# Optimization experiments

Hardware: AMD Instinct MI355X
Metric: run time of the kernel (lower is better)

Reference implementation:

```python
import jax, jax.numpy as jnp
import numpy as np

DIM = 1024
NUM_HEADS = 8
HEAD_DIM = 64
QK_DIM = NUM_HEADS * HEAD_DIM  # 512
B, S = 4, 1024


def setup_inputs() -> dict:
    key = jax.random.key(0)
    k1, k2, k3, k4, k5 = jax.random.split(key, 5)
    x = jax.random.normal(k1, (B, S, DIM), dtype=jnp.float32)
    mask = jax.random.randint(k2, (B, S), 0, 2).astype(bool)
    rotator = jax.random.normal(k3, (B, S, HEAD_DIM, HEAD_DIM), dtype=jnp.float32)
    # Linear weights stored as [in, out] for x @ W
    w_t = jax.random.normal(k4, (DIM, 2 * QK_DIM + DIM), dtype=jnp.float32) * (DIM ** -0.5)
    w_o = jax.random.normal(k5, (DIM, DIM), dtype=jnp.float32) * (DIM ** -0.5)
    return {"x": x, "mask": mask, "rotator": rotator, "w_t": w_t, "w_o": w_o}


def taylor_atn_fn(qs, ks, vs, mask):
    # 2nd-order Taylor approximation of softmax attention:
    # exp(s) ~= 1 + s + s^2/2, with invalid keys masked out.
    scale = HEAD_DIM ** -0.5
    s = jnp.einsum('bqhd,bkhd->bhqk', qs, ks) * scale  # [B,H,S,S]
    scores = 1.0 + s + 0.5 * s * s
    scores = scores * mask[:, None, None, :].astype(scores.dtype)  # mask keys
    denom = jnp.maximum(jnp.sum(scores, axis=-1), 1e-6)            # [B,H,Q]
    out = jnp.einsum('bhqk,bkhd->bqhd', scores, vs)
    out = out / jnp.transpose(denom, (0, 2, 1))[..., None]         # [B,Q,H,vd]
    return out.reshape(out.shape[0], out.shape[1], -1)


def reference(x, mask, rotator, w_t, w_o):
    t = x @ w_t                                   # [B,S,2*QK+DIM]
    Bx, Sx = t.shape[0], t.shape[1]
    qs = t[..., :QK_DIM].reshape(Bx, Sx, NUM_HEADS, HEAD_DIM)
    ks = t[..., QK_DIM:2 * QK_DIM].reshape(Bx, Sx, NUM_HEADS, HEAD_DIM)
    vs = t[..., 2 * QK_DIM:].reshape(Bx, Sx, NUM_HEADS, -1)
    m = mask[..., None, None]
    # masked per-position rotation: q -> R q, k -> R^T k
    qs = jnp.where(m, jnp.einsum('bsij,bshj->bshi', rotator, qs), qs)
    ks = jnp.where(m, jnp.einsum('bsij,bshi->bshj', rotator, ks), ks)
    out = taylor_atn_fn(qs, ks, vs, mask)
    return out @ w_o
```

## Files before the change

### kernel.cpp

```cpp
#include <hip/hip_runtime.h>
#include <cstdint>
#include <cstddef>

#define DIMX  1024
#define NH    8
#define HD    64
#define QKD   512
#define VDD   128
#define BATCH 4
#define SEQ   1024
#define NPOS  (BATCH*SEQ)
#define TW    (2*QKD + DIMX)
#define SCALE 0.125f

typedef __bf16 bf16x8 __attribute__((ext_vector_type(8)));
typedef float  f32x4  __attribute__((ext_vector_type(4)));
typedef float  f32x16 __attribute__((ext_vector_type(16)));

__device__ __forceinline__ ushort f2bf(float f) {
    unsigned b = __float_as_uint(f);
    return (ushort)((b + 0x7FFFu + ((b >> 16) & 1u)) >> 16);
}
__device__ __forceinline__ float bf2f(ushort u) {
    return __uint_as_float((unsigned)u << 16);
}

__device__ __forceinline__ unsigned cvtpk(float lo, float hi) {
    unsigned r;
    asm("v_cvt_pk_bf16_f32 %0, %1, %2" : "=v"(r) : "v"(lo), "v"(hi));
    return r;
}

__device__ __forceinline__ void plswap(unsigned &a, unsigned &b) {
    asm("v_permlane32_swap_b32 %0, %1" : "+v"(a), "+v"(b));
}

#define GLD16(src, dst) __builtin_amdgcn_global_load_lds(                      \
    (const __attribute__((address_space(1))) unsigned int*)(src),              \
    (__attribute__((address_space(3))) unsigned int*)(dst), 16, 0, 0)

#define SW(row, col) ((row)*64 + ((col) ^ (((row)&7)<<3)))

__device__ __forceinline__ int2 xcd_swz(int gx, int gy) {
    const int nwg = gx * gy;
    int id = blockIdx.y * gx + blockIdx.x;
    id = (id & 7) * (nwg >> 3) + (id >> 3);
    return make_int2(id % gx, id / gx);
}

__global__ __launch_bounds__(256)
void prep_all(const float* __restrict__ x, const float* __restrict__ w_t,
              const float* __restrict__ w_o, ushort* __restrict__ xbf,
              ushort* __restrict__ wtT, ushort* __restrict__ woT)
{
    __shared__ float tile[32][33];
    const int bid = blockIdx.x;
    if (bid < 2048) {
        const size_t i = ((size_t)bid * 256 + threadIdx.x) * 8;
        float4 v0 = *(const float4*)(x + i);
        float4 v1 = *(const float4*)(x + i + 4);
        ushort o[8] = {f2bf(v0.x), f2bf(v0.y), f2bf(v0.z), f2bf(v0.w),
                       f2bf(v1.x), f2bf(v1.y), f2bf(v1.z), f2bf(v1.w)};
        *(uint4*)(xbf + i) = *(uint4*)o;
        return;
    }
    const float* W; ushort* WT; int K, N, bn, bk;
    if (bid < 4096) {
        W = w_t; WT = wtT; K = DIMX; N = TW;
        const int t = bid - 2048;
        bn = (t & 63) * 32; bk = (t >> 6) * 32;
    } else {
        W = w_o; WT = woT; K = DIMX; N = DIMX;
        const int t = bid - 4096;
        bn = (t & 31) * 32; bk = (t >> 5) * 32;
    }
    const int tx = threadIdx.x & 31;
    const int ty = threadIdx.x >> 5;
    #pragma unroll
    for (int i = ty; i < 32; i += 8)
        tile[i][tx] = W[(size_t)(bk + i) * N + bn + tx];
    __syncthreads();
    #pragma unroll
    for (int i = ty; i < 32; i += 8)
        WT[(size_t)(bn + i) * K + bk + tx] = f2bf(tile[tx][i]);
}

#define GEMM_PROLOGUE(Aptr, Bptr, Kdim)                                        \
    __shared__ __align__(16) ushort lA[128 * 64];                              \
    __shared__ __align__(16) ushort lB[128 * 64];                              \
    const int tid  = threadIdx.x;                                              \
    const int lane = tid & 63;                                                 \
    const int wave = tid >> 6;                                                 \
    const int wr   = wave >> 1;                                                \
    const int wc   = wave & 1;                                                 \
    const int rsub = lane >> 3;                        \
    const int scol = ((lane & 7) * 8) ^ ((rsub & 7) << 3);                     \
    const ushort* aP = (Aptr) + (size_t)(bm + wave*32 + rsub) * (Kdim) + scol; \
    const ushort* bP = (Bptr) + (size_t)(bn + wave*32 + rsub) * (Kdim) + scol; \
    ushort* lAw = lA + wave * 2048;                                            \
    ushort* lBw = lB + wave * 2048;                                            \
    const int fr = lane & 15;                                                  \
    const int l4 = lane >> 4;                                                  \
    f32x4 acc[4][4] = {};

#define GEMM_KLOOP(Kdim)                                                       \
    for (int k0 = 0; k0 < (Kdim); k0 += 64) {                                  \
        _Pragma("unroll")                                                      \
        for (int c = 0; c < 4; ++c) {                                          \
            GLD16(aP + (size_t)(c*8) * (Kdim) + k0, lAw + c*512);              \
            GLD16(bP + (size_t)(c*8) * (Kdim) + k0, lBw + c*512);              \
        }                                                                      \
        asm volatile("s_waitcnt vmcnt(0)" ::: "memory");                       \
        __syncthreads();                                                       \
        _Pragma("unroll")                                                      \
        for (int ks = 0; ks < 2; ++ks) {                                       \
            bf16x8 af[4], bfr[4];                                              \
            _Pragma("unroll")                                                  \
            for (int m = 0; m < 4; ++m)                                        \
                af[m] = *(const bf16x8*)&lA[SW(wr*64 + m*16 + fr,              \
                                               ks*32 + l4*8)];                 \
            _Pragma("unroll")                                                  \
            for (int n = 0; n < 4; ++n)                                        \
                bfr[n] = *(const bf16x8*)&lB[SW(wc*64 + n*16 + fr,             \
                                                ks*32 + l4*8)];               \
            _Pragma("unroll")                                                  \
            for (int m = 0; m < 4; ++m)                                        \
                _Pragma("unroll")                                              \
                for (int n = 0; n < 4; ++n)                                    \
                    acc[m][n] = __builtin_amdgcn_mfma_f32_16x16x32_bf16(       \
                        af[m], bfr[n], acc[m][n], 0, 0, 0);                    \
        }                                                                      \
        __syncthreads();                                                       \
    }

__global__ __launch_bounds__(256, 2)
void gemm_qkv(const ushort* __restrict__ A, const ushort* __restrict__ BT,
              ushort* __restrict__ t1b, ushort* __restrict__ Vt)
{
    const int2 bij = xcd_swz(TW/128, NPOS/128);
    const int bm = bij.y * 128;
    const int bn = bij.x * 128;
    GEMM_PROLOGUE(A, BT, DIMX)
    GEMM_KLOOP(DIMX)

    const int orow = l4 * 4;
    if (bn < 1024) {
        #pragma unroll
        for (int m = 0; m < 4; ++m)
            #pragma unroll
            for (int n = 0; n < 4; ++n) {
                ushort* dst = t1b + (size_t)(bm + wr * 64 + m * 16 + orow) * 1024
                                  + bn + wc * 64 + n * 16 + fr;
                #pragma unroll
                for (int q = 0; q < 4; ++q)
                    dst[(size_t)q * 1024] = f2bf(acc[m][n][q]);
            }
    } else {
        #pragma unroll
        for (int m = 0; m < 4; ++m)
            #pragma unroll
            for (int n = 0; n < 4; ++n) {
                const int row0 = bm + wr * 64 + m * 16 + orow;
                const int cv   = bn + wc * 64 + n * 16 + fr - 1024;
                const int hh = cv >> 7, vd = cv & 127;
                const int bb = row0 >> 10, ss = row0 & 1023;
                ushort o4[4];
                #pragma unroll
                for (int q = 0; q < 4; ++q) o4[q] = f2bf(acc[m][n][q]);
                *(ushort4*)&Vt[((size_t)(bb*NH + hh)*VDD + vd)*SEQ + ss] =
                    *(ushort4*)o4;
            }
    }
}

__global__ __launch_bounds__(256, 2)
void gemm_bf16_mfma(const ushort* __restrict__ A, const ushort* __restrict__ BT,
                    float* __restrict__ C)
{
    const int2 bij = xcd_swz(DIMX/128, NPOS/128);
    const int bm = bij.y * 128;
    const int bn = bij.x * 128;
    GEMM_PROLOGUE(A, BT, DIMX)
    GEMM_KLOOP(DIMX)

    const int orow = l4 * 4;
    #pragma unroll
    for (int m = 0; m < 4; ++m)
        #pragma unroll
        for (int n = 0; n < 4; ++n) {
            float* dst = C + (size_t)(bm + wr * 64 + m * 16 + orow) * DIMX
                           + bn + wc * 64 + n * 16 + fr;
            #pragma unroll
            for (int q = 0; q < 4; ++q)
                dst[(size_t)q * DIMX] = acc[m][n][q];
        }
}

__global__ __launch_bounds__(256)
void rotate_pack_qk(const ushort* __restrict__ t1b, const int* __restrict__ mask,
                    const float* __restrict__ rot, ushort* __restrict__ Qb,
                    ushort* __restrict__ Kb)
{
    const int p   = blockIdx.x;
    const int tid = threadIdx.x;
    const int b = p >> 10, s = p & 1023;
    const bool rotated = (mask[p] != 0);

    __shared__ float R[64][69];
    __shared__ float qv[QKD];
    __shared__ float kv[QKD];

    const ushort* tq = t1b + (size_t)p * 1024;
    {
        ushort2 q2 = *(const ushort2*)(tq + tid*2);
        ushort2 k2 = *(const ushort2*)(tq + QKD + tid*2);
        qv[tid*2]   = bf2f(q2.x); qv[tid*2+1] = bf2f(q2.y);
        kv[tid*2]   = bf2f(k2.x); kv[tid*2+1] = bf2f(k2.y);
        if (rotated) {
            const float* Rg = rot + (size_t)p * 4096;
            const int base = tid * 16;
            const int r = base >> 6, c = base & 63;
            #pragma unroll
            for (int x = 0; x < 16; x += 4) {
                float4 v = *(const float4*)(Rg + base + x);
                R[r][c+x+0] = v.x; R[r][c+x+1] = v.y;
                R[r][c+x+2] = v.z; R[r][c+x+3] = v.w;
            }
        }
    }
    __syncthreads();

    #pragma unroll
    for (int ph = 0; ph < 2; ++ph) {
        const int h = (tid >> 6) + ph*4;
        const int i = tid & 63;
        const float* qh  = &qv[h*64];
        const float* kh2 = &kv[h*64];
        float aq, ak;
        if (rotated) {
            aq = 0.f; ak = 0.f;
            #pragma unroll 8
            for (int j = 0; j < 64; ++j) {
                aq = fmaf(R[i][j], qh[j], aq);
                ak = fmaf(R[j][i], kh2[j], ak);
            }
        } else {
            aq = qh[i]; ak = kh2[i];
        }
        const size_t dst = ((size_t)(b*NH + h)*SEQ + s)*HD + i;
        Qb[dst] = f2bf(aq * SCALE);
        Kb[dst] = f2bf(ak);
    }
}

__global__ __launch_bounds__(256, 2)
void taylor_attn_mfma(const ushort* __restrict__ Qb, const ushort* __restrict__ Kb,
                      const ushort* __restrict__ Vt, const int* __restrict__ mask,
                      ushort* __restrict__ attn)
{
    const int bh  = blockIdx.x;
    const int qt  = blockIdx.y;
    const int b   = bh >> 3, h = bh & 7;
    const int tid = threadIdx.x;
    const int lane = tid & 63;
    const int wave = tid >> 6;
    const int kh  = wave >> 1;
    const int qg  = wave & 1;
    const int l31 = lane & 31;
    const int g   = lane >> 5;

    __shared__ __align__(16) ushort smem[32768];
    __shared__ float mskAll[SEQ];
    __shared__ float dpart[64];
    __shared__ float dinv2[64];

    ushort* Ksp = smem + kh * 8192;
    ushort* Vsp = smem + 16384 + kh * 8192;
    float*  comb = (float*)smem;

    {
        int4 mv = *(const int4*)(mask + b*SEQ + tid*4);
        float4 f = make_float4(mv.x ? 1.f : 0.f, mv.y ? 1.f : 0.f,
                               mv.z ? 1.f : 0.f, mv.w ? 1.f : 0.f);
        *(float4*)&mskAll[tid*4] = f;
    }

    const ushort* qrow = Qb + ((size_t)bh*SEQ + qt*64 + qg*32 + l31) * HD + g*8;
    bf16x8 qf[4];
    #pragma unroll
    for (int ds = 0; ds < 4; ++ds) qf[ds] = *(const bf16x8*)(qrow + ds*16);

    const int sub  = lane >> 3;
    const int scol = ((lane & 7) * 8) ^ (sub << 3);
    const ushort* Kbase = Kb + (size_t)bh*SEQ*HD;
    const ushort* Vbase = Vt + (size_t)bh*VDD*SEQ;

#define ISSUE_K(buf, ktn) do {                                                 \
    _Pragma("unroll")                                                          \
    for (int i_ = 0; i_ < 4; ++i_)                                             \
        GLD16(Kbase + ((size_t)(ktn)*64 + 8*(qg*4+i_) + sub)*HD + scol,        \
              Ksp + (buf)*4096 + (qg*4+i_)*512);                               \
} while (0)
#define ISSUE_V(ktn) do {                                                      \
    _Pragma("unroll")                                                          \
    for (int i_ = 0; i_ < 8; ++i_)                                             \
        GLD16(Vbase + (size_t)(8*(qg*8+i_) + sub)*SEQ + (ktn)*64 + scol,       \
              Vsp + (qg*8+i_)*512);                                            \
} while (0)

    f32x16 acc[4] = {};
    float dacc = 0.f;

    __syncthreads();
    ISSUE_K(0, kh*8);

    for (int it = 0; it < 8; ++it) {
        const int kt = kh*8 + it;
        const int cb = it & 1;
        ISSUE_V(kt);
        if (it < 7) {
            ISSUE_K(cb ^ 1, kt + 1);
            asm volatile("s_waitcnt vmcnt(12)" ::: "memory");
        } else {
            asm volatile("s_waitcnt vmcnt(8)"  ::: "memory");
        }
        __builtin_amdgcn_s_barrier();

        f32x16 sf0 = {}, sf1 = {};
        __builtin_amdgcn_s_setprio(1);
        #pragma unroll
        for (int ds = 0; ds < 4; ++ds) {
            const int dc = ds*16 + g*8;
            bf16x8 kf0 = *(const bf16x8*)&Ksp[cb*4096 + SW(l31, dc)];
            bf16x8 kf1 = *(const bf16x8*)&Ksp[cb*4096 + SW(32 + l31, dc)];
            sf0 = __builtin_amdgcn_mfma_f32_32x32x16_bf16(kf0, qf[ds], sf0, 0, 0, 0);
            sf1 = __builtin_amdgcn_mfma_f32_32x32x16_bf16(kf1, qf[ds], sf1, 0, 0, 0);
        }
        __builtin_amdgcn_s_setprio(0);

        const float* mrow = mskAll + kt*64;
        unsigned w0[8], w1[8];
        float dadd = 0.f;
        #pragma unroll
        for (int rr = 0; rr < 4; ++rr) {
            const float4 mqa = *(const float4*)&mrow[8*rr + 4*g];
            const float4 mqb = *(const float4*)&mrow[32 + 8*rr + 4*g];
            float s0 = sf0[rr*4+0], s1 = sf0[rr*4+1];
            float s2 = sf0[rr*4+2], s3 = sf0[rr*4+3];
            float c0 = fmaf(fmaf(0.5f*s0, s0, s0), mqa.x, mqa.x);
            float c1 = fmaf(fmaf(0.5f*s1, s1, s1), mqa.y, mqa.y);
            float c2 = fmaf(fmaf(0.5f*s2, s2, s2), mqa.z, mqa.z);
            float c3 = fmaf(fmaf(0.5f*s3, s3, s3), mqa.w, mqa.w);
            float t0 = sf1[rr*4+0], t1 = sf1[rr*4+1];
            float t2 = sf1[rr*4+2], t3 = sf1[rr*4+3];
            float d0 = fmaf(fmaf(0.5f*t0, t0, t0), mqb.x, mqb.x);
            float d1 = fmaf(fmaf(0.5f*t1, t1, t1), mqb.y, mqb.y);
            float d2 = fmaf(fmaf(0.5f*t2, t2, t2), mqb.z, mqb.z);
            float d3 = fmaf(fmaf(0.5f*t3, t3, t3), mqb.w, mqb.w);
            dadd += ((c0+c1)+(c2+c3)) + ((d0+d1)+(d2+d3));
            w0[rr*2+0] = cvtpk(c0, c1);
            w0[rr*2+1] = cvtpk(c2, c3);
            w1[rr*2+0] = cvtpk(d0, d1);
            w1[rr*2+1] = cvtpk(d2, d3);
        }
        dacc += dadd;
        plswap(w0[0], w0[2]); plswap(w0[1], w0[3]);
        plswap(w0[4], w0[6]); plswap(w0[5], w0[7]);
        plswap(w1[0], w1[2]); plswap(w1[1], w1[3]);
        plswap(w1[4], w1[6]); plswap(w1[5], w1[7]);

        if (it < 7) asm volatile("s_waitcnt vmcnt(4)" ::: "memory");
        else        asm volatile("s_waitcnt vmcnt(0)" ::: "memory");
        __builtin_amdgcn_s_barrier();

        __builtin_amdgcn_s_setprio(1);
        #pragma unroll
        for (int kq = 0; kq < 4; ++kq) {
            union { unsigned u[4]; bf16x8 v; } pu;
            if (kq == 0)      { pu.u[0]=w0[0]; pu.u[1]=w0[1]; pu.u[2]=w0[2]; pu.u[3]=w0[3]; }
            else if (kq == 1) { pu.u[0]=w0[4]; pu.u[1]=w0[5]; pu.u[2]=w0[6]; pu.u[3]=w0[7]; }
            else if (kq == 2) { pu.u[0]=w1[0]; pu.u[1]=w1[1]; pu.u[2]=w1[2]; pu.u[3]=w1[3]; }
            else              { pu.u[0]=w1[4]; pu.u[1]=w1[5]; pu.u[2]=w1[6]; pu.u[3]=w1[7]; }
            const int kcol = kq*16 + g*8;
            acc[0] = __builtin_amdgcn_mfma_f32_32x32x16_bf16(
                pu.v, *(const bf16x8*)&Vsp[SW(      l31, kcol)], acc[0], 0, 0, 0);
            acc[1] = __builtin_amdgcn_mfma_f32_32x32x16_bf16(
                pu.v, *(const bf16x8*)&Vsp[SW( 32 + l31, kcol)], acc[1], 0, 0, 0);
            acc[2] = __builtin_amdgcn_mfma_f32_32x32x16_bf16(
                pu.v, *(const bf16x8*)&Vsp[SW( 64 + l31, kcol)], acc[2], 0, 0, 0);
            acc[3] = __builtin_amdgcn_mfma_f32_32x32x16_bf16(
                pu.v, *(const bf16x8*)&Vsp[SW( 96 + l31, kcol)], acc[3], 0, 0, 0);
        }
        __builtin_amdgcn_s_setprio(0);
        __builtin_amdgcn_s_barrier();
    }
#undef ISSUE_K
#undef ISSUE_V

    const float dhalf = dacc + __shfl_xor(dacc, 32);

    if (kh == 1) {
        float* cbp = comb + qg * 4096;
        #pragma unroll
        for (int vb = 0; vb < 4; ++vb)
            #pragma unroll
            for (int rr = 0; rr < 4; ++rr) {
                float4 v = make_float4(acc[vb][rr*4+0], acc[vb][rr*4+1],
                                       acc[vb][rr*4+2], acc[vb][rr*4+3]);
                *(float4*)&cbp[(vb*32 + l31)*32 + 4*g + 8*rr] = v;
            }
        if (lane < 32) dpart[qg*32 + l31] = dhalf;
    }
    __syncthreads();
    if (kh == 0) {
        float* cbp = comb + qg * 4096;
        const float dtot = dhalf + dpart[qg*32 + l31];
        if (lane < 32) dinv2[qg*32 + l31] = 1.f / fmaxf(dtot, 1e-6f);
        #pragma unroll
        for (int vb = 0; vb < 4; ++vb)
            #pragma unroll
            for (int rr = 0; rr < 4; ++rr) {
                float4 v = *(const float4*)&cbp[(vb*32 + l31)*32 + 4*g + 8*rr];
                acc[vb][rr*4+0] += v.x; acc[vb][rr*4+1] += v.y;
                acc[vb][rr*4+2] += v.z; acc[vb][rr*4+3] += v.w;
            }
        float inv[16];
        #pragma unroll
        for (int rr = 0; rr < 4; ++rr) {
            float4 iv = *(const float4*)&dinv2[qg*32 + 8*rr + 4*g];
            inv[rr*4+0] = iv.x; inv[rr*4+1] = iv.y;
            inv[rr*4+2] = iv.z; inv[rr*4+3] = iv.w;
        }
        ushort* obase = attn + ((size_t)(b*SEQ + qt*64 + qg*32)) * DIMX
                      + h*VDD + l31;
        #pragma unroll
        for (int vb = 0; vb < 4; ++vb)
            #pragma unroll
            for (int rr = 0; rr < 4; ++rr)
                #pragma unroll
                for (int j = 0; j < 4; ++j) {
                    const int q = 4*g + 8*rr + j;
                    obase[(size_t)q*DIMX + vb*32] = f2bf(acc[vb][rr*4+j] * inv[rr*4+j]);
                }
    }
}

extern "C" void kernel_launch(void* const* d_in, const int* in_sizes, int n_in,
                              void* d_out, int out_size, void* d_ws, size_t ws_size,
                              hipStream_t stream)
{
    const float* x    = (const float*)d_in[0];
    const int*   mask = (const int*)d_in[1];
    const float* rot  = (const float*)d_in[2];
    const float* w_t  = (const float*)d_in[3];
    const float* w_o  = (const float*)d_in[4];
    float* out = (float*)d_out;

    ushort* t1b    = (ushort*)d_ws;
    ushort* xbf    = t1b + (size_t)NPOS * 1024;
    ushort* attnbf = xbf;
    ushort* wtT    = xbf + (size_t)NPOS * DIMX;
    ushort* woT    = wtT + (size_t)TW * DIMX;
    ushort* Qb     = woT + (size_t)DIMX * DIMX;
    ushort* Kb     = Qb  + (size_t)BATCH * NH * SEQ * HD;
    ushort* Vtp    = Kb  + (size_t)BATCH * NH * SEQ * HD;

    prep_all<<<5120, 256, 0, stream>>>(x, w_t, w_o, xbf, wtT, woT);

    gemm_qkv<<<dim3(TW/128, NPOS/128), 256, 0, stream>>>(xbf, wtT, t1b, Vtp);
    rotate_pack_qk<<<NPOS, 256, 0, stream>>>(t1b, mask, rot, Qb, Kb);
    taylor_attn_mfma<<<dim3(BATCH*NH, SEQ/64), 256, 0, stream>>>(Qb, Kb, Vtp, mask, attnbf);
    gemm_bf16_mfma<<<dim3(DIMX/128, NPOS/128), 256, 0, stream>>>(attnbf, woT, out);
}
```

Before: 98.34 us.

## Give each wave private K/V LDS tiles to remove per-iteration workgroup barriers

Result: slower. 101.4 us (+3.2%).

```diff
diff --git a/kernel.cpp b/kernel.cpp
--- a/kernel.cpp
+++ b/kernel.cpp
@@ -40,6 +40,7 @@
     (__attribute__((address_space(3))) unsigned int*)(dst), 16, 0, 0)
 
 #define SW(row, col) ((row)*64 + ((col) ^ (((row)&7)<<3)))
+#define SW32(row, col) ((row)*32 + ((col) ^ ((((row)>>1)&3)<<3)))
 
 __device__ __forceinline__ int2 xcd_swz(int gx, int gy) {
     const int nwg = gx * gy;
@@ -274,8 +275,8 @@
     __shared__ float dpart[64];
     __shared__ float dinv2[64];
 
-    ushort* Ksp = smem + kh * 8192;
-    ushort* Vsp = smem + 16384 + kh * 8192;
+    ushort* Ksp = smem + wave * 8192;
+    ushort* Vsp = Ksp + 4096;
     float*  comb = (float*)smem;
 
     {
@@ -290,114 +291,99 @@
     #pragma unroll
     for (int ds = 0; ds < 4; ++ds) qf[ds] = *(const bf16x8*)(qrow + ds*16);
 
-    const int sub  = lane >> 3;
-    const int scol = ((lane & 7) * 8) ^ (sub << 3);
+    const int ksub  = lane >> 3;
+    const int kcolS = ((lane & 7) * 8) ^ (ksub << 3);
+    const int vrow  = lane >> 2;
+    const int vcolS = ((lane & 3) * 8) ^ (((lane >> 3) & 3) << 3);
     const ushort* Kbase = Kb + (size_t)bh*SEQ*HD;
     const ushort* Vbase = Vt + (size_t)bh*VDD*SEQ;
 
 #define ISSUE_K(buf, ktn) do {                                                 \
     _Pragma("unroll")                                                          \
     for (int i_ = 0; i_ < 4; ++i_)                                             \
-        GLD16(Kbase + ((size_t)(ktn)*64 + 8*(qg*4+i_) + sub)*HD + scol,        \
-              Ksp + (buf)*4096 + (qg*4+i_)*512);                               \
+        GLD16(Kbase + ((size_t)(ktn)*32 + 8*i_ + ksub)*HD + kcolS,             \
+              Ksp + (buf)*2048 + i_*512);                                      \
 } while (0)
 #define ISSUE_V(ktn) do {                                                      \
     _Pragma("unroll")                                                          \
     for (int i_ = 0; i_ < 8; ++i_)                                             \
-        GLD16(Vbase + (size_t)(8*(qg*8+i_) + sub)*SEQ + (ktn)*64 + scol,       \
-              Vsp + (qg*8+i_)*512);                                            \
+        GLD16(Vbase + (size_t)(16*i_ + vrow)*SEQ + (ktn)*32 + vcolS,           \
+              Vsp + i_*512);                                                   \
 } while (0)
 
     f32x16 acc[4] = {};
     float dacc = 0.f;
 
     __syncthreads();
-    ISSUE_K(0, kh*8);
-
-    for (int it = 0; it < 8; ++it) {
-        const int kt = kh*8 + it;
+    ISSUE_K(0, kh*16);
+
+    for (int it = 0; it < 16; ++it) {
+        const int kt = kh*16 + it;
         const int cb = it & 1;
+        asm volatile("s_waitcnt lgkmcnt(0)" ::: "memory");
         ISSUE_V(kt);
-        if (it < 7) {
+        if (it < 15) {
             ISSUE_K(cb ^ 1, kt + 1);
             asm volatile("s_waitcnt vmcnt(12)" ::: "memory");
         } else {
             asm volatile("s_waitcnt vmcnt(8)"  ::: "memory");
         }
-        __builtin_amdgcn_s_barrier();
-
-        f32x16 sf0 = {}, sf1 = {};
+
+        f32x16 sf0 = {};
         __builtin_amdgcn_s_setprio(1);
         #pragma unroll
         for (int ds = 0; ds < 4; ++ds) {
-            const int dc = ds*16 + g*8;
-            bf16x8 kf0 = *(const bf16x8*)&Ksp[cb*4096 + SW(l31, dc)];
-            bf16x8 kf1 = *(const bf16x8*)&Ksp[cb*4096 + SW(32 + l31, dc)];
-            sf0 = __builtin_amdgcn_mfma_f32_32x32x16_bf16(kf0, qf[ds], sf0, 0, 0, 0);
-            sf1 = __builtin_amdgcn_mfma_f32_32x32x16_bf16(kf1, qf[ds], sf1, 0, 0, 0);
+            bf16x8 kf = *(const bf16x8*)&Ksp[cb*2048 + SW(l31, ds*16 + g*8)];
+            sf0 = __builtin_amdgcn_mfma_f32_32x32x16_bf16(kf, qf[ds], sf0, 0, 0, 0);
         }
         __builtin_amdgcn_s_setprio(0);
 
-        const float* mrow = mskAll + kt*64;
-        unsigned w0[8], w1[8];
+        const float* mrow = mskAll + kt*32;
+        unsigned w[8];
         float dadd = 0.f;
         #pragma unroll
         for (int rr = 0; rr < 4; ++rr) {
-            const float4 mqa = *(const float4*)&mrow[8*rr + 4*g];
-            const float4 mqb = *(const float4*)&mrow[32 + 8*rr + 4*g];
+            const float4 mq = *(const float4*)&mrow[8*rr + 4*g];
             float s0 = sf0[rr*4+0], s1 = sf0[rr*4+1];
             float s2 = sf0[rr*4+2], s3 = sf0[rr*4+3];
-            float c0 = fmaf(fmaf(0.5f*s0, s0, s0), mqa.x, mqa.x);
-            float c1 = fmaf(fmaf(0.5f*s1, s1, s1), mqa.y, mqa.y);
-            float c2 = fmaf(fmaf(0.5f*s2, s2, s2), mqa.z, mqa.z);
-            float c3 = fmaf(fmaf(0.5f*s3, s3, s3), mqa.w, mqa.w);
-            float t0 = sf1[rr*4+0], t1 = sf1[rr*4+1];
-            float t2 = sf1[rr*4+2], t3 = sf1[rr*4+3];
-            float d0 = fmaf(fmaf(0.5f*t0, t0, t0), mqb.x, mqb.x);
-            float d1 = fmaf(fmaf(0.5f*t1, t1, t1), mqb.y, mqb.y);
-            float d2 = fmaf(fmaf(0.5f*t2, t2, t2), mqb.z, mqb.z);
-            float d3 = fmaf(fmaf(0.5f*t3, t3, t3), mqb.w, mqb.w);
-            dadd += ((c0+c1)+(c2+c3)) + ((d0+d1)+(d2+d3));
-            w0[rr*2+0] = cvtpk(c0, c1);
-            w0[rr*2+1] = cvtpk(c2, c3);
-            w1[rr*2+0] = cvtpk(d0, d1);
-            w1[rr*2+1] = cvtpk(d2, d3);
+            float c0 = fmaf(fmaf(0.5f*s0, s0, s0), mq.x, mq.x);
+            float c1 = fmaf(fmaf(0.5f*s1, s1, s1), mq.y, mq.y);
+            float c2 = fmaf(fmaf(0.5f*s2, s2, s2), mq.z, mq.z);
+            float c3 = fmaf(fmaf(0.5f*s3, s3, s3), mq.w, mq.w);
+            dadd += (c0 + c1) + (c2 + c3);
+            w[rr*2+0] = cvtpk(c0, c1);
+            w[rr*2+1] = cvtpk(c2, c3);
         }
         dacc += dadd;
-        plswap(w0[0], w0[2]); plswap(w0[1], w0[3]);
-        plswap(w0[4], w0[6]); plswap(w0[5], w0[7]);
-        plswap(w1[0], w1[2]); plswap(w1[1], w1[3]);
-        plswap(w1[4], w1[6]); plswap(w1[5], w1[7]);
-
-        if (it < 7) asm volatile("s_waitcnt vmcnt(4)" ::: "memory");
-        else        asm volatile("s_waitcnt vmcnt(0)" ::: "memory");
-        __builtin_amdgcn_s_barrier();
+        plswap(w[0], w[2]); plswap(w[1], w[3]);
+        plswap(w[4], w[6]); plswap(w[5], w[7]);
+
+        if (it < 15) asm volatile("s_waitcnt vmcnt(4)" ::: "memory");
+        else         asm volatile("s_waitcnt vmcnt(0)" ::: "memory");
 
         __builtin_amdgcn_s_setprio(1);
         #pragma unroll
-        for (int kq = 0; kq < 4; ++kq) {
+        for (int kq = 0; kq < 2; ++kq) {
             union { unsigned u[4]; bf16x8 v; } pu;
-            if (kq == 0)      { pu.u[0]=w0[0]; pu.u[1]=w0[1]; pu.u[2]=w0[2]; pu.u[3]=w0[3]; }
-            else if (kq == 1) { pu.u[0]=w0[4]; pu.u[1]=w0[5]; pu.u[2]=w0[6]; pu.u[3]=w0[7]; }
-            else if (kq == 2) { pu.u[0]=w1[0]; pu.u[1]=w1[1]; pu.u[2]=w1[2]; pu.u[3]=w1[3]; }
-            else              { pu.u[0]=w1[4]; pu.u[1]=w1[5]; pu.u[2]=w1[6]; pu.u[3]=w1[7]; }
+            if (kq == 0) { pu.u[0]=w[0]; pu.u[1]=w[1]; pu.u[2]=w[2]; pu.u[3]=w[3]; }
+            else         { pu.u[0]=w[4]; pu.u[1]=w[5]; pu.u[2]=w[6]; pu.u[3]=w[7]; }
             const int kcol = kq*16 + g*8;
             acc[0] = __builtin_amdgcn_mfma_f32_32x32x16_bf16(
-                pu.v, *(const bf16x8*)&Vsp[SW(      l31, kcol)], acc[0], 0, 0, 0);
+                pu.v, *(const bf16x8*)&Vsp[SW32(      l31, kcol)], acc[0], 0, 0, 0);
             acc[1] = __builtin_amdgcn_mfma_f32_32x32x16_bf16(
-                pu.v, *(const bf16x8*)&Vsp[SW( 32 + l31, kcol)], acc[1], 0, 0, 0);
+                pu.v, *(const bf16x8*)&Vsp[SW32( 32 + l31, kcol)], acc[1], 0, 0, 0);
             acc[2] = __builtin_amdgcn_mfma_f32_32x32x16_bf16(
-                pu.v, *(const bf16x8*)&Vsp[SW( 64 + l31, kcol)], acc[2], 0, 0, 0);
+                pu.v, *(const bf16x8*)&Vsp[SW32( 64 + l31, kcol)], acc[2], 0, 0, 0);
             acc[3] = __builtin_amdgcn_mfma_f32_32x32x16_bf16(
-                pu.v, *(const bf16x8*)&Vsp[SW( 96 + l31, kcol)], acc[3], 0, 0, 0);
+                pu.v, *(const bf16x8*)&Vsp[SW32( 96 + l31, kcol)], acc[3], 0, 0, 0);
         }
         __builtin_amdgcn_s_setprio(0);
-        __builtin_amdgcn_s_barrier();
     }
 #undef ISSUE_K
 #undef ISSUE_V
 
     const float dhalf = dacc + __shfl_xor(dacc, 32);
+    __syncthreads();
 
     if (kh == 1) {
         float* cbp = comb + qg * 4096;
```

## Double-buffer LDS tiles in GEMM k-loop to overlap global loads with MFMA

Applied to the files above, without the earlier changes.

After: 97.38 us. About the same (-1.0%).

```diff
diff --git a/kernel.cpp b/kernel.cpp
--- a/kernel.cpp
+++ b/kernel.cpp
@@ -86,8 +86,8 @@
 }
 
 #define GEMM_PROLOGUE(Aptr, Bptr, Kdim)                                        \
-    __shared__ __align__(16) ushort lA[128 * 64];                              \
-    __shared__ __align__(16) ushort lB[128 * 64];                              \
+    __shared__ __align__(16) ushort lA[2 * 128 * 64];                          \
+    __shared__ __align__(16) ushort lB[2 * 128 * 64];                          \
     const int tid  = threadIdx.x;                                              \
     const int lane = tid & 63;                                                 \
     const int wave = tid >> 6;                                                 \
@@ -103,26 +103,37 @@
     const int l4 = lane >> 4;                                                  \
     f32x4 acc[4][4] = {};
 
-#define GEMM_KLOOP(Kdim)                                                       \
-    for (int k0 = 0; k0 < (Kdim); k0 += 64) {                                  \
+#define GSTAGE(buf, k0, Kdim)                                                  \
+    do {                                                                       \
         _Pragma("unroll")                                                      \
         for (int c = 0; c < 4; ++c) {                                          \
-            GLD16(aP + (size_t)(c*8) * (Kdim) + k0, lAw + c*512);              \
-            GLD16(bP + (size_t)(c*8) * (Kdim) + k0, lBw + c*512);              \
+            GLD16(aP + (size_t)(c*8) * (Kdim) + (k0), lAw + (buf)*8192 + c*512);\
+            GLD16(bP + (size_t)(c*8) * (Kdim) + (k0), lBw + (buf)*8192 + c*512);\
         }                                                                      \
-        asm volatile("s_waitcnt vmcnt(0)" ::: "memory");                       \
-        __syncthreads();                                                       \
+    } while (0)
+
+#define GEMM_KLOOP(Kdim)                                                       \
+    GSTAGE(0, 0, Kdim);                                                        \
+    for (int t = 0; t < (Kdim)/64; ++t) {                                      \
+        const int cur = t & 1;                                                 \
+        if (t < (Kdim)/64 - 1) {                                               \
+            GSTAGE(cur ^ 1, (t + 1) * 64, Kdim);                               \
+            asm volatile("s_waitcnt vmcnt(8)" ::: "memory");                   \
+        } else {                                                               \
+            asm volatile("s_waitcnt vmcnt(0)" ::: "memory");                   \
+        }                                                                      \
+        __builtin_amdgcn_s_barrier();               \
         _Pragma("unroll")                                                      \
         for (int ks = 0; ks < 2; ++ks) {                                       \
             bf16x8 af[4], bfr[4];                                              \
             _Pragma("unroll")                                                  \
             for (int m = 0; m < 4; ++m)                                        \
-                af[m] = *(const bf16x8*)&lA[SW(wr*64 + m*16 + fr,              \
-                                               ks*32 + l4*8)];                 \
+                af[m] = *(const bf16x8*)&lA[cur*8192 +                         \
+                    SW(wr*64 + m*16 + fr, ks*32 + l4*8)];                      \
             _Pragma("unroll")                                                  \
             for (int n = 0; n < 4; ++n)                                        \
-                bfr[n] = *(const bf16x8*)&lB[SW(wc*64 + n*16 + fr,             \
-                                                ks*32 + l4*8)];               \
+                bfr[n] = *(const bf16x8*)&lB[cur*8192 +                        \
+                    SW(wc*64 + n*16 + fr, ks*32 + l4*8)];                      \
             _Pragma("unroll")                                                  \
             for (int m = 0; m < 4; ++m)                                        \
                 _Pragma("unroll")                                              \
@@ -130,7 +141,8 @@
                     acc[m][n] = __builtin_amdgcn_mfma_f32_16x16x32_bf16(       \
                         af[m], bfr[n], acc[m][n], 0, 0, 0);                    \
         }                                                                      \
-        __syncthreads();                                                       \
+        asm volatile("s_waitcnt lgkmcnt(0)" ::: "memory");                     \
+        __builtin_amdgcn_s_barrier();             \
     }
 
 __global__ __launch_bounds__(256, 2)
```
